# Performance work log

Measured on AMD Instinct MI355X. Metric: run time of the kernel, lower is better.

## Reference

```python
import jax, jax.numpy as jnp
import numpy as np

N = 100000   # nodes
E = 1600000  # edges
EL = 1000000 # label edges
F = 64       # node_features (== LSTM hidden)
S = 64       # second_features
C = 32       # num_classes


def setup_inputs() -> dict:
    key = jax.random.key(0)
    ks = jax.random.split(key, 11)
    sc = 0.05
    return {
        "x": jax.random.normal(ks[0], (N, F), jnp.float32),
        "edge_index": jax.random.randint(ks[1], (2, E), 0, N, jnp.int32),
        "edge_label_index": jax.random.randint(ks[2], (2, EL), 0, N, jnp.int32),
        "W_ih": jax.random.normal(ks[3], (4 * F, F), jnp.float32) * sc,
        "W_hh": jax.random.normal(ks[4], (4 * F, F), jnp.float32) * sc,
        "b_ih": jax.random.normal(ks[5], (4 * F,), jnp.float32) * sc,
        "b_hh": jax.random.normal(ks[6], (4 * F,), jnp.float32) * sc,
        "W1": jax.random.normal(ks[7], (F, S), jnp.float32) * sc,
        "b1": jnp.zeros((S,), jnp.float32),
        "W2": jax.random.normal(ks[8], (S, C), jnp.float32) * sc,
        "b2": jnp.zeros((C,), jnp.float32),
    }


def lstm_step(x, W_ih, W_hh, b_ih, b_hh):
    # seq_len == 1, h0 = c0 = 0, so W_hh contributes nothing but both biases apply.
    gates = x @ W_ih.T + b_ih + b_hh          # [N, 4F], PyTorch gate order i,f,g,o
    i, f, g, o = jnp.split(gates, 4, axis=-1)
    c = jax.nn.sigmoid(i) * jnp.tanh(g)
    return jax.nn.sigmoid(o) * jnp.tanh(c)    # [N, F]


def gcn_conv(h, W, b, row, col, n):
    # PyG GCNConv default: add self-loops, symmetric normalization.
    hw = h @ W                                 # [n, out]
    loop = jnp.arange(n, dtype=row.dtype)
    row_sl = jnp.concatenate([row, loop])
    col_sl = jnp.concatenate([col, loop])
    deg = jax.ops.segment_sum(jnp.ones_like(col_sl, jnp.float32), col_sl, num_segments=n)
    dinv = jnp.where(deg > 0, jax.lax.rsqrt(deg), 0.0)
    norm = dinv[row_sl] * dinv[col_sl]         # [E+n]
    msgs = hw[row_sl] * norm[:, None]          # gather + scale
    out = jax.ops.segment_sum(msgs, col_sl, num_segments=n)  # scatter-add
    return out + b


def reference(x, edge_index, edge_label_index, W_ih, W_hh, b_ih, b_hh, W1, b1, W2, b2):
    n = x.shape[0]
    row, col = edge_index[0], edge_index[1]
    h = lstm_step(x, W_ih, W_hh, b_ih, b_hh)
    h = jax.nn.relu(gcn_conv(h, W1, b1, row, col, n))
    z = gcn_conv(h, W2, b2, row, col, n)       # [n, C]
    src = z[edge_label_index[0]]
    dst = z[edge_label_index[1]]
    return jnp.sum(src * dst, axis=-1)         # [EL]
```

## Files before the change

### kernel.cpp

```cpp
#include <hip/hip_runtime.h>
#include <hip/hip_bf16.h>
#include <hip/hip_fp16.h>
#include <math.h>
#include <stdint.h>

#define NBSH 9
#define CH   4096

typedef _Float16 h2v  __attribute__((ext_vector_type(2)));
typedef _Float16 half8 __attribute__((ext_vector_type(8)));
typedef float    f32x4 __attribute__((ext_vector_type(4)));

__device__ __forceinline__ float fdot2_(unsigned a, unsigned b, float c) {
    return __builtin_amdgcn_fdot2(__builtin_bit_cast(h2v, a),
                                  __builtin_bit_cast(h2v, b), c, false);
}

__device__ __forceinline__ float2 h2f2_(unsigned u) {
    return __half22float2(__builtin_bit_cast(__half2, u));
}

__device__ __forceinline__ float fast_sigmoid(float x) {
    float t = __expf(x);
    return 1.0f - __builtin_amdgcn_rcpf(1.0f + t);
}
__device__ __forceinline__ float fast_tanh(float x) {
    float t = __expf(2.0f * x);
    return 1.0f - 2.0f * __builtin_amdgcn_rcpf(1.0f + t);
}

__global__ __launch_bounds__(256) void k_bhist(const int* __restrict__ col,
        int* __restrict__ bdeg, int E, int nbuck) {
    __shared__ int cnt[256];
    cnt[threadIdx.x] = 0;
    __syncthreads();
    int base = blockIdx.x * CH;
    int end  = base + CH; if (end > E) end = E;
    for (int t = base + (int)threadIdx.x; t < end; t += 256)
        atomicAdd(&cnt[col[t] >> NBSH], 1);
    __syncthreads();
    if ((int)threadIdx.x < nbuck && cnt[threadIdx.x] > 0)
        atomicAdd(&bdeg[threadIdx.x], cnt[threadIdx.x]);
}

__global__ __launch_bounds__(256) void k_bscan(const int* __restrict__ bdeg,
        int* __restrict__ boff, int* __restrict__ gcur, int nbuck, int E) {
    __shared__ int tmp[256];
    int tid = threadIdx.x;
    int v = (tid < nbuck) ? bdeg[tid] : 0;
    tmp[tid] = v;
    __syncthreads();
#pragma unroll
    for (int s = 1; s < 256; s <<= 1) {
        int t = (tid >= s) ? tmp[tid - s] : 0;
        __syncthreads();
        tmp[tid] += t;
        __syncthreads();
    }
    if (tid < nbuck) {
        int o = tmp[tid] - v;
        boff[tid] = o;
        gcur[tid * 16] = o;
    }
    if (tid == 0) boff[nbuck] = E;
}

__global__ __launch_bounds__(256) void k_bin(
    const int* __restrict__ row, const int* __restrict__ col,
    int* __restrict__ gcur, int2* __restrict__ ebuf, int E, int nbuck)
{
    __shared__ int  cnt[256], lofs[256], gbase[256], cur2[256];
    __shared__ int2 stage[CH];
    int tid  = threadIdx.x;
    int base = blockIdx.x * CH;
    int ned  = E - base; if (ned > CH) ned = CH;

    cnt[tid] = 0;
    __syncthreads();

    int r[16], c[16], b[16];
#pragma unroll
    for (int i = 0; i < 16; i++) {
        int idx = i * 256 + tid;
        if (idx < ned) {
            r[i] = row[base + idx];
            c[i] = col[base + idx];
            b[i] = c[i] >> NBSH;
            atomicAdd(&cnt[b[i]], 1);
        } else { r[i] = 0; c[i] = 0; b[i] = -1; }
    }
    __syncthreads();

    int v = cnt[tid];
    lofs[tid] = v;
    __syncthreads();
#pragma unroll
    for (int s = 1; s < 256; s <<= 1) {
        int t = (tid >= s) ? lofs[tid - s] : 0;
        __syncthreads();
        lofs[tid] += t;
        __syncthreads();
    }
    int excl = lofs[tid] - v;
    __syncthreads();
    lofs[tid] = excl;
    cur2[tid] = excl;
    if (tid < nbuck && v > 0)
        gbase[tid] = atomicAdd(&gcur[tid * 16], v);
    __syncthreads();

#pragma unroll
    for (int i = 0; i < 16; i++) {
        if (b[i] >= 0) {
            int p = atomicAdd(&cur2[b[i]], 1);
            stage[p] = make_int2(r[i], c[i]);
        }
    }
    __syncthreads();

    for (int i = tid; i < ned; i += 256) {
        int2 rc = stage[i];
        int bb = rc.y >> NBSH;
        ebuf[gbase[bb] + (i - lofs[bb])] = rc;
    }
}

__global__ __launch_bounds__(512) void k_csr(
    const int2* __restrict__ ebuf, const int* __restrict__ boff,
    int* __restrict__ off, float* __restrict__ dinv,
    int* __restrict__ nbr, int n, int nbuck, int E)
{
    __shared__ int cnt[512], lofs[512];
    int b   = blockIdx.x;
    int tid = threadIdx.x;
    int c0  = b << NBSH;
    int nn  = n - c0; if (nn > 512) nn = 512; if (nn < 0) nn = 0;
    int lo  = boff[b], hi = boff[b + 1];

    cnt[tid] = 0;
    __syncthreads();
    for (int t = lo + tid; t < hi; t += 512)
        atomicAdd(&cnt[ebuf[t].y & 511], 1);
    __syncthreads();

    int v = cnt[tid];
    lofs[tid] = v;
    __syncthreads();
#pragma unroll
    for (int s = 1; s < 512; s <<= 1) {
        int t = (tid >= s) ? lofs[tid - s] : 0;
        __syncthreads();
        lofs[tid] += t;
        __syncthreads();
    }
    int excl = lofs[tid] - v;
    __syncthreads();

    if (tid < nn) {
        off[c0 + tid]  = lo + excl;
        dinv[c0 + tid] = 1.0f / sqrtf((float)(v + 1));
    }
    if (b == nbuck - 1 && tid == 0) off[n] = E;

    cnt[tid] = excl;
    __syncthreads();
    for (int t = lo + tid; t < hi; t += 512) {
        int2 rc = ebuf[t];
        int p = atomicAdd(&cnt[rc.y & 511], 1);
        nbr[lo + p] = rc.x;
    }
}

__global__ void k_tr(const float* __restrict__ Wih, const float* __restrict__ W1,
                     const float* __restrict__ bih, const float* __restrict__ bhh,
                     uint4* __restrict__ B1tab, uint4* __restrict__ B2tab,
                     float* __restrict__ bsum) {
    int t = blockIdx.x * 256 + threadIdx.x;
    if (t < 1536) {
        int e = t >> 6, l = t & 63;
        int tt = e >> 1, kh = e & 1;
        int gate = tt >> 2, tj = tt & 3;
        int j = 16 * tj + (l & 15);
        int rowb = (gate == 0) ? j : (gate == 1) ? (128 + j) : (192 + j);
        int kbase = kh * 32 + 8 * (l >> 4);
        _Float16 v[8];
#pragma unroll
        for (int jj = 0; jj < 8; jj++)
            v[jj] = (_Float16)Wih[rowb * 64 + kbase + jj];
        B1tab[t] = *reinterpret_cast<uint4*>(v);
    } else if (t < 2048) {
        int u = t - 1536;
        int e = u >> 6, l = u & 63;
        int tt = e >> 1, kh = e & 1;
        int s = 16 * tt + (l & 15);
        int kbase = kh * 32 + 8 * (l >> 4);
        _Float16 v[8];
#pragma unroll
        for (int jj = 0; jj < 8; jj++)
            v[jj] = (_Float16)W1[(kbase + jj) * 64 + s];
        B2tab[u] = *reinterpret_cast<uint4*>(v);
    } else if (t < 2240) {
        int c = t - 2048;
        int gate = c >> 6, j = c & 63;
        int rowb = (gate == 0) ? j : (gate == 1) ? (128 + j) : (192 + j);
        bsum[c] = bih[rowb] + bhh[rowb];
    }
}

__global__ __launch_bounds__(256) void k_lstm_mm1(
    const float* __restrict__ x, const uint4* __restrict__ B1tab,
    const uint4* __restrict__ B2tab, const float* __restrict__ bsum,
    __half* __restrict__ hw1, int n)
{
    __shared__ _Float16 hs[4][16 * 72];
    int wv   = threadIdx.x >> 6;
    int lane = threadIdx.x & 63;
    int nbase = (blockIdx.x * 4 + wv) * 16;
    if (nbase >= n) return;
    int m16 = lane & 15, q = lane >> 4;

    int node = nbase + m16; if (node >= n) node = n - 1;
    const float* xr = x + (size_t)node * 64 + 8 * q;
    half8 a0, a1;
#pragma unroll
    for (int jj = 0; jj < 8; jj++) a0[jj] = (_Float16)xr[jj];
#pragma unroll
    for (int jj = 0; jj < 8; jj++) a1[jj] = (_Float16)xr[32 + jj];

    f32x4 c1[12];
#pragma unroll
    for (int t = 0; t < 12; t++) {
        f32x4 acc = {0.f, 0.f, 0.f, 0.f};
        half8 b0 = __builtin_bit_cast(half8, B1tab[(t * 2 + 0) * 64 + lane]);
        half8 b1 = __builtin_bit_cast(half8, B1tab[(t * 2 + 1) * 64 + lane]);
        acc = __builtin_amdgcn_mfma_f32_16x16x32_f16(a0, b0, acc, 0, 0, 0);
        acc = __builtin_amdgcn_mfma_f32_16x16x32_f16(a1, b1, acc, 0, 0, 0);
        c1[t] = acc;
    }

#pragma unroll
    for (int tj = 0; tj < 4; tj++) {
        int j = 16 * tj + m16;
        float bi = bsum[j], bg = bsum[64 + j], bo = bsum[128 + j];
#pragma unroll
        for (int r = 0; r < 4; r++) {
            float gi = c1[tj][r]     + bi;
            float gg = c1[4 + tj][r] + bg;
            float go = c1[8 + tj][r] + bo;
            float cc = fast_sigmoid(gi) * fast_tanh(gg);
            float h  = fast_sigmoid(go) * fast_tanh(cc);
            hs[wv][(q * 4 + r) * 72 + j] = (_Float16)h;
        }
    }

    half8 a20 = __builtin_bit_cast(half8,
        *reinterpret_cast<const uint4*>(&hs[wv][m16 * 72 + 8 * q]));
    half8 a21 = __builtin_bit_cast(half8,
        *reinterpret_cast<const uint4*>(&hs[wv][m16 * 72 + 32 + 8 * q]));

    f32x4 c2[4];
#pragma unroll
    for (int t = 0; t < 4; t++) {
        f32x4 acc = {0.f, 0.f, 0.f, 0.f};
        half8 b0 = __builtin_bit_cast(half8, B2tab[(t * 2 + 0) * 64 + lane]);
        half8 b1 = __builtin_bit_cast(half8, B2tab[(t * 2 + 1) * 64 + lane]);
        acc = __builtin_amdgcn_mfma_f32_16x16x32_f16(a20, b0, acc, 0, 0, 0);
        acc = __builtin_amdgcn_mfma_f32_16x16x32_f16(a21, b1, acc, 0, 0, 0);
        c2[t] = acc;
    }

#pragma unroll
    for (int t = 0; t < 4; t++) {
#pragma unroll
        for (int r = 0; r < 4; r++) {
            int nd = nbase + q * 4 + r;
            if (nd < n)
                hw1[(size_t)nd * 64 + 16 * t + m16] = __float2half(c2[t][r]);
        }
    }
}

__global__ __launch_bounds__(256) void k_pull64(
    const __half* __restrict__ hw, const int* __restrict__ off,
    const int* __restrict__ nbr, const float* __restrict__ dinv,
    const float* __restrict__ b1, float* __restrict__ h1, int n)
{
    int w    = (blockIdx.x * 256 + threadIdx.x) >> 6;
    int lane = threadIdx.x & 63;
    int quad = lane >> 4;
    int fp   = lane & 15;
    if (w * 4 >= n) return;
    int node = w * 4 + quad;
    bool alive = node < n;
    int s = 0, e = 0;
    if (alive) { s = off[node]; e = off[node + 1]; }

    float s0x=0.f,s0y=0.f,s0z=0.f,s0w=0.f;
    float s1x=0.f,s1y=0.f,s1z=0.f,s1w=0.f;
    float s2x=0.f,s2y=0.f,s2z=0.f,s2w=0.f;
    float s3x=0.f,s3y=0.f,s3z=0.f,s3w=0.f;

    for (int base = s; base < e; base += 16) {
        int t = base + fp;
        int idx = 0; float wv = 0.f;
        if (t < e) { idx = nbr[t]; wv = dinv[idx]; }
        int cnt = e - base; if (cnt > 16) cnt = 16;

        int k = 0;
        for (; k + 4 <= cnt; k += 4) {
            int   r0 = __shfl(idx, k + 0, 16); float w0 = __shfl(wv, k + 0, 16);
            int   r1 = __shfl(idx, k + 1, 16); float w1 = __shfl(wv, k + 1, 16);
            int   r2 = __shfl(idx, k + 2, 16); float w2 = __shfl(wv, k + 2, 16);
            int   r3 = __shfl(idx, k + 3, 16); float w3 = __shfl(wv, k + 3, 16);
            uint2 u0 = reinterpret_cast<const uint2*>(hw + (size_t)r0 * 64)[fp];
            uint2 u1 = reinterpret_cast<const uint2*>(hw + (size_t)r1 * 64)[fp];
            uint2 u2 = reinterpret_cast<const uint2*>(hw + (size_t)r2 * 64)[fp];
            uint2 u3 = reinterpret_cast<const uint2*>(hw + (size_t)r3 * 64)[fp];
            float2 l0 = h2f2_(u0.x), h0 = h2f2_(u0.y);
            float2 l1 = h2f2_(u1.x), h1f = h2f2_(u1.y);
            float2 l2 = h2f2_(u2.x), h2 = h2f2_(u2.y);
            float2 l3 = h2f2_(u3.x), h3 = h2f2_(u3.y);
            s0x = fmaf(l0.x, w0, s0x); s0y = fmaf(l0.y, w0, s0y);
            s0z = fmaf(h0.x, w0, s0z); s0w = fmaf(h0.y, w0, s0w);
            s1x = fmaf(l1.x, w1, s1x); s1y = fmaf(l1.y, w1, s1y);
            s1z = fmaf(h1f.x, w1, s1z); s1w = fmaf(h1f.y, w1, s1w);
            s2x = fmaf(l2.x, w2, s2x); s2y = fmaf(l2.y, w2, s2y);
            s2z = fmaf(h2.x, w2, s2z); s2w = fmaf(h2.y, w2, s2w);
            s3x = fmaf(l3.x, w3, s3x); s3y = fmaf(l3.y, w3, s3y);
            s3z = fmaf(h3.x, w3, s3z); s3w = fmaf(h3.y, w3, s3w);
        }
        for (; k < cnt; k++) {
            int   r0 = __shfl(idx, k, 16);
            float w0 = __shfl(wv, k, 16);
            uint2 u0 = reinterpret_cast<const uint2*>(hw + (size_t)r0 * 64)[fp];
            float2 l0 = h2f2_(u0.x), h0 = h2f2_(u0.y);
            s0x = fmaf(l0.x, w0, s0x); s0y = fmaf(l0.y, w0, s0y);
            s0z = fmaf(h0.x, w0, s0z); s0w = fmaf(h0.y, w0, s0w);
        }
    }

    if (alive) {
        float ax = (s0x + s1x) + (s2x + s3x);
        float ay = (s0y + s1y) + (s2y + s3y);
        float az = (s0z + s1z) + (s2z + s3z);
        float aw = (s0w + s1w) + (s2w + s3w);
        float dc = dinv[node];
        uint2 su = reinterpret_cast<const uint2*>(hw + (size_t)node * 64)[fp];
        float2 sl = h2f2_(su.x), sh = h2f2_(su.y);
        float4 bb = reinterpret_cast<const float4*>(b1)[fp];
        float vx = fmaxf(ax * dc + sl.x * dc * dc + bb.x, 0.0f);
        float vy = fmaxf(ay * dc + sl.y * dc * dc + bb.y, 0.0f);
        float vz = fmaxf(az * dc + sh.x * dc * dc + bb.z, 0.0f);
        float vw = fmaxf(aw * dc + sh.y * dc * dc + bb.w, 0.0f);
        reinterpret_cast<float4*>(h1 + (size_t)node * 64)[fp] =
            make_float4(vx, vy, vz, vw);
    }
}

__global__ __launch_bounds__(256) void k_pull32(
    const __half* __restrict__ hw, const int* __restrict__ off,
    const int* __restrict__ nbr, const float* __restrict__ dinv,
    const float* __restrict__ b2, __half* __restrict__ z, int n)
{
    int w    = (blockIdx.x * 256 + threadIdx.x) >> 6;
    int lane = threadIdx.x & 63;
    int quad = lane >> 4;
    int fp   = lane & 15;
    if (w * 4 >= n) return;
    int node = w * 4 + quad;
    bool alive = node < n;
    int s = 0, e = 0;
    if (alive) { s = off[node]; e = off[node + 1]; }

    float ax0 = 0.f, ay0 = 0.f, ax1 = 0.f, ay1 = 0.f;
    float ax2 = 0.f, ay2 = 0.f, ax3 = 0.f, ay3 = 0.f;

    for (int base = s; base < e; base += 16) {
        int t = base + fp;
        int idx = 0; float wv = 0.f;
        if (t < e) { idx = nbr[t]; wv = dinv[idx]; }
        int cnt = e - base; if (cnt > 16) cnt = 16;

        int k = 0;
        for (; k + 4 <= cnt; k += 4) {
            int   r0 = __shfl(idx, k + 0, 16); float w0 = __shfl(wv, k + 0, 16);
            int   r1 = __shfl(idx, k + 1, 16); float w1 = __shfl(wv, k + 1, 16);
            int   r2 = __shfl(idx, k + 2, 16); float w2 = __shfl(wv, k + 2, 16);
            int   r3 = __shfl(idx, k + 3, 16); float w3 = __shfl(wv, k + 3, 16);
            unsigned u0 = reinterpret_cast<const unsigned*>(hw + (size_t)r0 * 32)[fp];
            unsigned u1 = reinterpret_cast<const unsigned*>(hw + (size_t)r1 * 32)[fp];
            unsigned u2 = reinterpret_cast<const unsigned*>(hw + (size_t)r2 * 32)[fp];
            unsigned u3 = reinterpret_cast<const unsigned*>(hw + (size_t)r3 * 32)[fp];
            float2 f0 = h2f2_(u0), f1 = h2f2_(u1), f2 = h2f2_(u2), f3 = h2f2_(u3);
            ax0 = fmaf(f0.x, w0, ax0); ay0 = fmaf(f0.y, w0, ay0);
            ax1 = fmaf(f1.x, w1, ax1); ay1 = fmaf(f1.y, w1, ay1);
            ax2 = fmaf(f2.x, w2, ax2); ay2 = fmaf(f2.y, w2, ay2);
            ax3 = fmaf(f3.x, w3, ax3); ay3 = fmaf(f3.y, w3, ay3);
        }
        for (; k < cnt; k++) {
            int   r0 = __shfl(idx, k, 16);
            float w0 = __shfl(wv, k, 16);
            unsigned u0 = reinterpret_cast<const unsigned*>(hw + (size_t)r0 * 32)[fp];
            float2 f0 = h2f2_(u0);
            ax0 = fmaf(f0.x, w0, ax0); ay0 = fmaf(f0.y, w0, ay0);
        }
    }

    if (alive) {
        float ax = (ax0 + ax1) + (ax2 + ax3);
        float ay = (ay0 + ay1) + (ay2 + ay3);
        float dc = dinv[node];
        unsigned su = reinterpret_cast<const unsigned*>(hw + (size_t)node * 32)[fp];
        float2 sf = h2f2_(su);
        float2 bb = reinterpret_cast<const float2*>(b2)[fp];
        float vx = ax * dc + sf.x * dc * dc + bb.x;
        float vy = ay * dc + sf.y * dc * dc + bb.y;
        __half2 pk(__float2half(vx), __float2half(vy));
        reinterpret_cast<__half2*>(z + (size_t)node * 32)[fp] = pk;
    }
}

__global__ __launch_bounds__(128) void k_mm2(
    const float* __restrict__ h1, const float* __restrict__ W2,
    __half* __restrict__ hw2, int n)
{
    __shared__ float tile[128 * 65];
    int base  = blockIdx.x * 128;
    int nrows = n - base; if (nrows > 128) nrows = 128;

    for (int idx = threadIdx.x; idx < nrows * 64; idx += 128) {
        int r = idx >> 6, c = idx & 63;
        tile[r * 65 + c] = h1[(size_t)base * 64 + idx];
    }
    __syncthreads();

    int node = base + threadIdx.x;
    if (node >= n) return;

    const float* hrow = &tile[threadIdx.x * 65];
    float acc[32];
#pragma unroll
    for (int s = 0; s < 32; s++) acc[s] = 0.0f;

    for (int k = 0; k < 64; k++) {
        float hk = hrow[k];
        const float* w = W2 + (size_t)k * 32;
#pragma unroll
        for (int s = 0; s < 32; s++) acc[s] = fmaf(hk, w[s], acc[s]);
    }

    uint2* op = reinterpret_cast<uint2*>(hw2 + (size_t)node * 32);
#pragma unroll
    for (int q = 0; q < 8; q++) {
        __half2 lo(__float2half(acc[4*q+0]), __float2half(acc[4*q+1]));
        __half2 hi(__float2half(acc[4*q+2]), __float2half(acc[4*q+3]));
        op[q] = make_uint2(__builtin_bit_cast(unsigned, lo),
                           __builtin_bit_cast(unsigned, hi));
    }
}

__global__ void k_dot(const __half* __restrict__ z, const int* __restrict__ src,
                      const int* __restrict__ dst, float* __restrict__ out, int EL)
{
    int e = blockIdx.x * 256 + threadIdx.x;
    if (e >= EL) return;
    const uint4* a = reinterpret_cast<const uint4*>(z + (size_t)src[e] * 32);
    const uint4* b = reinterpret_cast<const uint4*>(z + (size_t)dst[e] * 32);
    float s = 0.0f;
#pragma unroll
    for (int q = 0; q < 4; q++) {
        uint4 av = a[q], bv = b[q];
        s = fdot2_(av.x, bv.x, s);
        s = fdot2_(av.y, bv.y, s);
        s = fdot2_(av.z, bv.z, s);
        s = fdot2_(av.w, bv.w, s);
    }
    out[e] = s;
}

extern "C" void kernel_launch(void* const* d_in, const int* in_sizes, int n_in,
                              void* d_out, int out_size, void* d_ws, size_t ws_size,
                              hipStream_t stream)
{
    const float* x   = (const float*)d_in[0];
    const int*   ei  = (const int*)d_in[1];
    const int*   eli = (const int*)d_in[2];
    const float* Wih = (const float*)d_in[3];
    const float* bih = (const float*)d_in[5];
    const float* bhh = (const float*)d_in[6];
    const float* W1  = (const float*)d_in[7];
    const float* b1  = (const float*)d_in[8];
    const float* W2  = (const float*)d_in[9];
    const float* b2  = (const float*)d_in[10];

    int n  = in_sizes[0] / 64;
    int E  = in_sizes[1] / 2;
    int EL = in_sizes[2] / 2;

    const int* row  = ei;
    const int* col  = ei + E;
    const int* lsrc = eli;
    const int* ldst = eli + EL;
    float* out = (float*)d_out;

    float*    bufA  = (float*)d_ws;
    float*    bufB  = bufA + (size_t)n * 64;
    float*    dinv  = bufB + (size_t)n * 64;
    uintptr_t pal   = ((uintptr_t)(dinv + n) + 15) & ~(uintptr_t)15;
    uint4*    B1tab = (uint4*)pal;
    uint4*    B2tab = B1tab + 1536;
    float*    bsum  = (float*)(B2tab + 512);
    int*      off   = (int*)(bsum + 192);
    int*      nbr   = off + (n + 1);
    int*      bdeg  = nbr + E;
    int*      boff  = bdeg + 256;
    int*      gcur  = boff + 257;
    int2*     ebuf  = (int2*)bufA;
    __half*   hw1h  = (__half*)bufA;
    __half*   hw2h  = (__half*)bufA;
    float*    h1    = bufB;
    __half*   zh    = (__half*)bufB;

    int nbuck   = (n + (1 << NBSH) - 1) >> NBSH;
    int eblocks = (E + CH - 1) / CH;
    dim3 blk(256);

    k_tr<<<dim3(9), blk, 0, stream>>>(Wih, W1, bih, bhh, B1tab, B2tab, bsum);

    hipMemsetAsync(bdeg, 0, 256 * sizeof(int), stream);
    k_bhist<<<dim3(eblocks), blk, 0, stream>>>(col, bdeg, E, nbuck);
    k_bscan<<<dim3(1), blk, 0, stream>>>(bdeg, boff, gcur, nbuck, E);
    k_bin  <<<dim3(eblocks), blk, 0, stream>>>(row, col, gcur, ebuf, E, nbuck);
    k_csr  <<<dim3(nbuck), dim3(512), 0, stream>>>(ebuf, boff, off, dinv, nbr, n, nbuck, E);

    {
        int blocks = (n + 63) / 64;
        k_lstm_mm1<<<dim3(blocks), blk, 0, stream>>>(x, B1tab, B2tab, bsum, hw1h, n);
    }

    {
        int blocks = (n + 15) / 16;
        k_pull64<<<dim3(blocks), blk, 0, stream>>>(hw1h, off, nbr, dinv, b1, h1, n);
    }

    k_mm2<<<dim3((n + 127) / 128), dim3(128), 0, stream>>>(h1, W2, hw2h, n);

    {
        int blocks = (n + 15) / 16;
        k_pull32<<<dim3(blocks), blk, 0, stream>>>(hw2h, off, nbr, dinv, b2, zh, n);
    }

    k_dot<<<dim3((EL + 255) / 256), blk, 0, stream>>>(zh, lsrc, ldst, out, EL);
}
```

Baseline: 198.6 us.

## Merge independent kernels into shared launches and store layer-1 output in fp16

Folds weight-table preparation into the bucket-histogram launch, and runs edge binning and the LSTM+first matmul as two block ranges of a single launch. This cuts launch count and lets independent work overlap on the GPU. The ReLU'd first-layer aggregate is now stored as fp16 instead of fp32, halving its write and its read in the second matmul. The workspace is re-laid out so ebuf no longer aliases the hw1 buffer. The trade-offs are extra precision loss in h1 and a larger shared-memory footprint for the merged binning/LSTM blocks.

```diff
diff --git a/kernel.cpp b/kernel.cpp
--- a/kernel.cpp
+++ b/kernel.cpp
@@ -29,12 +29,50 @@
     return 1.0f - 2.0f * __builtin_amdgcn_rcpf(1.0f + t);
 }
 
-__global__ __launch_bounds__(256) void k_bhist(const int* __restrict__ col,
-        int* __restrict__ bdeg, int E, int nbuck) {
+__global__ __launch_bounds__(256) void k_trh(
+    const float* __restrict__ Wih, const float* __restrict__ W1,
+    const float* __restrict__ bih, const float* __restrict__ bhh,
+    uint4* __restrict__ B1tab, uint4* __restrict__ B2tab,
+    float* __restrict__ bsum,
+    const int* __restrict__ col, int* __restrict__ bdeg, int E, int nbuck)
+{
+    if (blockIdx.x < 9) {
+        int t = blockIdx.x * 256 + threadIdx.x;
+        if (t < 1536) {
+            int e = t >> 6, l = t & 63;
+            int tt = e >> 1, kh = e & 1;
+            int gate = tt >> 2, tj = tt & 3;
+            int j = 16 * tj + (l & 15);
+            int rowb = (gate == 0) ? j : (gate == 1) ? (128 + j) : (192 + j);
+            int kbase = kh * 32 + 8 * (l >> 4);
+            _Float16 v[8];
+#pragma unroll
+            for (int jj = 0; jj < 8; jj++)
+                v[jj] = (_Float16)Wih[rowb * 64 + kbase + jj];
+            B1tab[t] = *reinterpret_cast<uint4*>(v);
+        } else if (t < 2048) {
+            int u = t - 1536;
+            int e = u >> 6, l = u & 63;
+            int tt = e >> 1, kh = e & 1;
+            int s = 16 * tt + (l & 15);
+            int kbase = kh * 32 + 8 * (l >> 4);
+            _Float16 v[8];
+#pragma unroll
+            for (int jj = 0; jj < 8; jj++)
+                v[jj] = (_Float16)W1[(kbase + jj) * 64 + s];
+            B2tab[u] = *reinterpret_cast<uint4*>(v);
+        } else if (t < 2240) {
+            int c = t - 2048;
+            int gate = c >> 6, j = c & 63;
+            int rowb = (gate == 0) ? j : (gate == 1) ? (128 + j) : (192 + j);
+            bsum[c] = bih[rowb] + bhh[rowb];
+        }
+        return;
+    }
     __shared__ int cnt[256];
     cnt[threadIdx.x] = 0;
     __syncthreads();
-    int base = blockIdx.x * CH;
+    int base = (blockIdx.x - 9) * CH;
     int end  = base + CH; if (end > E) end = E;
     for (int t = base + (int)threadIdx.x; t < end; t += 256)
         atomicAdd(&cnt[col[t] >> NBSH], 1);
@@ -65,159 +103,83 @@
     if (tid == 0) boff[nbuck] = E;
 }
 
-__global__ __launch_bounds__(256) void k_bin(
+__global__ __launch_bounds__(256) void k_binl(
     const int* __restrict__ row, const int* __restrict__ col,
-    int* __restrict__ gcur, int2* __restrict__ ebuf, int E, int nbuck)
-{
-    __shared__ int  cnt[256], lofs[256], gbase[256], cur2[256];
-    __shared__ int2 stage[CH];
-    int tid  = threadIdx.x;
-    int base = blockIdx.x * CH;
-    int ned  = E - base; if (ned > CH) ned = CH;
-
-    cnt[tid] = 0;
-    __syncthreads();
-
-    int r[16], c[16], b[16];
-#pragma unroll
-    for (int i = 0; i < 16; i++) {
-        int idx = i * 256 + tid;
-        if (idx < ned) {
-            r[i] = row[base + idx];
-            c[i] = col[base + idx];
-            b[i] = c[i] >> NBSH;
-            atomicAdd(&cnt[b[i]], 1);
-        } else { r[i] = 0; c[i] = 0; b[i] = -1; }
-    }
-    __syncthreads();
-
-    int v = cnt[tid];
-    lofs[tid] = v;
-    __syncthreads();
-#pragma unroll
-    for (int s = 1; s < 256; s <<= 1) {
-        int t = (tid >= s) ? lofs[tid - s] : 0;
-        __syncthreads();
-        lofs[tid] += t;
-        __syncthreads();
-    }
-    int excl = lofs[tid] - v;
-    __syncthreads();
-    lofs[tid] = excl;
-    cur2[tid] = excl;
-    if (tid < nbuck && v > 0)
-        gbase[tid] = atomicAdd(&gcur[tid * 16], v);
-    __syncthreads();
-
-#pragma unroll
-    for (int i = 0; i < 16; i++) {
-        if (b[i] >= 0) {
-            int p = atomicAdd(&cur2[b[i]], 1);
-            stage[p] = make_int2(r[i], c[i]);
-        }
-    }
-    __syncthreads();
-
-    for (int i = tid; i < ned; i += 256) {
-        int2 rc = stage[i];
-        int bb = rc.y >> NBSH;
-        ebuf[gbase[bb] + (i - lofs[bb])] = rc;
-    }
-}
-
-__global__ __launch_bounds__(512) void k_csr(
-    const int2* __restrict__ ebuf, const int* __restrict__ boff,
-    int* __restrict__ off, float* __restrict__ dinv,
-    int* __restrict__ nbr, int n, int nbuck, int E)
-{
-    __shared__ int cnt[512], lofs[512];
-    int b   = blockIdx.x;
-    int tid = threadIdx.x;
-    int c0  = b << NBSH;
-    int nn  = n - c0; if (nn > 512) nn = 512; if (nn < 0) nn = 0;
-    int lo  = boff[b], hi = boff[b + 1];
-
-    cnt[tid] = 0;
-    __syncthreads();
-    for (int t = lo + tid; t < hi; t += 512)
-        atomicAdd(&cnt[ebuf[t].y & 511], 1);
-    __syncthreads();
-
-    int v = cnt[tid];
-    lofs[tid] = v;
-    __syncthreads();
-#pragma unroll
-    for (int s = 1; s < 512; s <<= 1) {
-        int t = (tid >= s) ? lofs[tid - s] : 0;
-        __syncthreads();
-        lofs[tid] += t;
-        __syncthreads();
-    }
-    int excl = lofs[tid] - v;
-    __syncthreads();
-
-    if (tid < nn) {
-        off[c0 + tid]  = lo + excl;
-        dinv[c0 + tid] = 1.0f / sqrtf((float)(v + 1));
-    }
-    if (b == nbuck - 1 && tid == 0) off[n] = E;
-
-    cnt[tid] = excl;
-    __syncthreads();
-    for (int t = lo + tid; t < hi; t += 512) {
-        int2 rc = ebuf[t];
-        int p = atomicAdd(&cnt[rc.y & 511], 1);
-        nbr[lo + p] = rc.x;
-    }
-}
-
-__global__ void k_tr(const float* __restrict__ Wih, const float* __restrict__ W1,
-                     const float* __restrict__ bih, const float* __restrict__ bhh,
-                     uint4* __restrict__ B1tab, uint4* __restrict__ B2tab,
-                     float* __restrict__ bsum) {
-    int t = blockIdx.x * 256 + threadIdx.x;
-    if (t < 1536) {
-        int e = t >> 6, l = t & 63;
-        int tt = e >> 1, kh = e & 1;
-        int gate = tt >> 2, tj = tt & 3;
-        int j = 16 * tj + (l & 15);
-        int rowb = (gate == 0) ? j : (gate == 1) ? (128 + j) : (192 + j);
-        int kbase = kh * 32 + 8 * (l >> 4);
-        _Float16 v[8];
-#pragma unroll
-        for (int jj = 0; jj < 8; jj++)
-            v[jj] = (_Float16)Wih[rowb * 64 + kbase + jj];
-        B1tab[t] = *reinterpret_cast<uint4*>(v);
-    } else if (t < 2048) {
-        int u = t - 1536;
-        int e = u >> 6, l = u & 63;
-        int tt = e >> 1, kh = e & 1;
-        int s = 16 * tt + (l & 15);
-        int kbase = kh * 32 + 8 * (l >> 4);
-        _Float16 v[8];
-#pragma unroll
-        for (int jj = 0; jj < 8; jj++)
-            v[jj] = (_Float16)W1[(kbase + jj) * 64 + s];
-        B2tab[u] = *reinterpret_cast<uint4*>(v);
-    } else if (t < 2240) {
-        int c = t - 2048;
-        int gate = c >> 6, j = c & 63;
-        int rowb = (gate == 0) ? j : (gate == 1) ? (128 + j) : (192 + j);
-        bsum[c] = bih[rowb] + bhh[rowb];
-    }
-}
-
-__global__ __launch_bounds__(256) void k_lstm_mm1(
+    int* __restrict__ gcur, int2* __restrict__ ebuf, int E, int nbuck,
+    int eblocks,
     const float* __restrict__ x, const uint4* __restrict__ B1tab,
     const uint4* __restrict__ B2tab, const float* __restrict__ bsum,
     __half* __restrict__ hw1, int n)
 {
-    __shared__ _Float16 hs[4][16 * 72];
+    __shared__ int pool[9216];
+    if ((int)blockIdx.x < eblocks) {
+        int* cnt  = pool;
+        int* lofs = pool + 256;
+        int* gbase = pool + 512;
+        int* cur2 = pool + 768;
+        int2* stage = (int2*)(pool + 1024);
+        int tid  = threadIdx.x;
+        int base = blockIdx.x * CH;
+        int ned  = E - base; if (ned > CH) ned = CH;
+
+        cnt[tid] = 0;
+        __syncthreads();
+
+        int r[16], c[16], b[16];
+#pragma unroll
+        for (int i = 0; i < 16; i++) {
+            int idx = i * 256 + tid;
+            if (idx < ned) {
+                r[i] = row[base + idx];
+                c[i] = col[base + idx];
+                b[i] = c[i] >> NBSH;
+                atomicAdd(&cnt[b[i]], 1);
+            } else { r[i] = 0; c[i] = 0; b[i] = -1; }
+        }
+        __syncthreads();
+
+        int v = cnt[tid];
+        lofs[tid] = v;
+        __syncthreads();
+#pragma unroll
+        for (int s = 1; s < 256; s <<= 1) {
+            int t = (tid >= s) ? lofs[tid - s] : 0;
+            __syncthreads();
+            lofs[tid] += t;
+            __syncthreads();
+        }
+        int excl = lofs[tid] - v;
+        __syncthreads();
+        lofs[tid] = excl;
+        cur2[tid] = excl;
+        if (tid < nbuck && v > 0)
+            gbase[tid] = atomicAdd(&gcur[tid * 16], v);
+        __syncthreads();
+
+#pragma unroll
+        for (int i = 0; i < 16; i++) {
+            if (b[i] >= 0) {
+                int p = atomicAdd(&cur2[b[i]], 1);
+                stage[p] = make_int2(r[i], c[i]);
+            }
+        }
+        __syncthreads();
+
+        for (int i = tid; i < ned; i += 256) {
+            int2 rc = stage[i];
+            int bb = rc.y >> NBSH;
+            ebuf[gbase[bb] + (i - lofs[bb])] = rc;
+        }
+        return;
+    }
+
+    _Float16* hsp = (_Float16*)pool;
     int wv   = threadIdx.x >> 6;
     int lane = threadIdx.x & 63;
-    int nbase = (blockIdx.x * 4 + wv) * 16;
+    int nbase = (((int)blockIdx.x - eblocks) * 4 + wv) * 16;
     if (nbase >= n) return;
     int m16 = lane & 15, q = lane >> 4;
+    _Float16* hs = hsp + wv * 1152;
 
     int node = nbase + m16; if (node >= n) node = n - 1;
     const float* xr = x + (size_t)node * 64 + 8 * q;
@@ -249,14 +211,14 @@
             float go = c1[8 + tj][r] + bo;
             float cc = fast_sigmoid(gi) * fast_tanh(gg);
             float h  = fast_sigmoid(go) * fast_tanh(cc);
-            hs[wv][(q * 4 + r) * 72 + j] = (_Float16)h;
+            hs[(q * 4 + r) * 72 + j] = (_Float16)h;
         }
     }
 
     half8 a20 = __builtin_bit_cast(half8,
-        *reinterpret_cast<const uint4*>(&hs[wv][m16 * 72 + 8 * q]));
+        *reinterpret_cast<const uint4*>(&hs[m16 * 72 + 8 * q]));
     half8 a21 = __builtin_bit_cast(half8,
-        *reinterpret_cast<const uint4*>(&hs[wv][m16 * 72 + 32 + 8 * q]));
+        *reinterpret_cast<const uint4*>(&hs[m16 * 72 + 32 + 8 * q]));
 
     f32x4 c2[4];
 #pragma unroll
@@ -280,10 +242,56 @@
     }
 }
 
+__global__ __launch_bounds__(512) void k_csr(
+    const int2* __restrict__ ebuf, const int* __restrict__ boff,
+    int* __restrict__ off, float* __restrict__ dinv,
+    int* __restrict__ nbr, int n, int nbuck, int E)
+{
+    __shared__ int cnt[512], lofs[512];
+    int b   = blockIdx.x;
+    int tid = threadIdx.x;
+    int c0  = b << NBSH;
+    int nn  = n - c0; if (nn > 512) nn = 512; if (nn < 0) nn = 0;
+    int lo  = boff[b], hi = boff[b + 1];
+
+    cnt[tid] = 0;
+    __syncthreads();
+    for (int t = lo + tid; t < hi; t += 512)
+        atomicAdd(&cnt[ebuf[t].y & 511], 1);
+    __syncthreads();
+
+    int v = cnt[tid];
+    lofs[tid] = v;
+    __syncthreads();
+#pragma unroll
+    for (int s = 1; s < 512; s <<= 1) {
+        int t = (tid >= s) ? lofs[tid - s] : 0;
+        __syncthreads();
+        lofs[tid] += t;
+        __syncthreads();
+    }
+    int excl = lofs[tid] - v;
+    __syncthreads();
+
+    if (tid < nn) {
+        off[c0 + tid]  = lo + excl;
+        dinv[c0 + tid] = 1.0f / sqrtf((float)(v + 1));
+    }
+    if (b == nbuck - 1 && tid == 0) off[n] = E;
+
+    cnt[tid] = excl;
+    __syncthreads();
+    for (int t = lo + tid; t < hi; t += 512) {
+        int2 rc = ebuf[t];
+        int p = atomicAdd(&cnt[rc.y & 511], 1);
+        nbr[lo + p] = rc.x;
+    }
+}
+
 __global__ __launch_bounds__(256) void k_pull64(
     const __half* __restrict__ hw, const int* __restrict__ off,
     const int* __restrict__ nbr, const float* __restrict__ dinv,
-    const float* __restrict__ b1, float* __restrict__ h1, int n)
+    const float* __restrict__ b1, __half* __restrict__ h1, int n)
 {
     int w    = (blockIdx.x * 256 + threadIdx.x) >> 6;
     int lane = threadIdx.x & 63;
@@ -352,8 +360,11 @@
         float vy = fmaxf(ay * dc + sl.y * dc * dc + bb.y, 0.0f);
         float vz = fmaxf(az * dc + sh.x * dc * dc + bb.z, 0.0f);
         float vw = fmaxf(aw * dc + sh.y * dc * dc + bb.w, 0.0f);
-        reinterpret_cast<float4*>(h1 + (size_t)node * 64)[fp] =
-            make_float4(vx, vy, vz, vw);
+        __half2 p0(__float2half(vx), __float2half(vy));
+        __half2 p1(__float2half(vz), __float2half(vw));
+        uint2 pk = make_uint2(__builtin_bit_cast(unsigned, p0),
+                              __builtin_bit_cast(unsigned, p1));
+        reinterpret_cast<uint2*>(h1 + (size_t)node * 64)[fp] = pk;
     }
 }
 
@@ -421,16 +432,19 @@
 }
 
 __global__ __launch_bounds__(128) void k_mm2(
-    const float* __restrict__ h1, const float* __restrict__ W2,
+    const __half* __restrict__ h1, const float* __restrict__ W2,
     __half* __restrict__ hw2, int n)
 {
     __shared__ float tile[128 * 65];
     int base  = blockIdx.x * 128;
     int nrows = n - base; if (nrows > 128) nrows = 128;
 
-    for (int idx = threadIdx.x; idx < nrows * 64; idx += 128) {
-        int r = idx >> 6, c = idx & 63;
-        tile[r * 65 + c] = h1[(size_t)base * 64 + idx];
+    for (int idx = threadIdx.x; idx < nrows * 32; idx += 128) {
+        int r = idx >> 5, c = idx & 31;
+        __half2 hv = reinterpret_cast<const __half2*>(h1 + (size_t)(base + r) * 64)[c];
+        float2 f = __half22float2(hv);
+        tile[r * 65 + 2 * c]     = f.x;
+        tile[r * 65 + 2 * c + 1] = f.y;
     }
     __syncthreads();
 
@@ -503,47 +517,47 @@
     const int* ldst = eli + EL;
     float* out = (float*)d_out;
 
-    float*    bufA  = (float*)d_ws;
-    float*    bufB  = bufA + (size_t)n * 64;
-    float*    dinv  = bufB + (size_t)n * 64;
-    uintptr_t pal   = ((uintptr_t)(dinv + n) + 15) & ~(uintptr_t)15;
+    float*    base  = (float*)d_ws;
+    int2*     ebuf  = (int2*)base;
+    __half*   hw2h  = (__half*)base;
+    float*    p1    = base + (size_t)E * 2;
+    __half*   hw1h  = (__half*)p1;
+    float*    p2    = p1 + (size_t)n * 32;
+    __half*   h1h   = (__half*)p2;
+    __half*   zh    = (__half*)p2;
+    float*    dinv  = p2 + (size_t)n * 32;
+    int*      off   = (int*)(dinv + n);
+    int*      nbr   = off + (n + 1);
+    uintptr_t pal   = ((uintptr_t)(nbr + E) + 15) & ~(uintptr_t)15;
     uint4*    B1tab = (uint4*)pal;
     uint4*    B2tab = B1tab + 1536;
     float*    bsum  = (float*)(B2tab + 512);
-    int*      off   = (int*)(bsum + 192);
-    int*      nbr   = off + (n + 1);
-    int*      bdeg  = nbr + E;
+    int*      bdeg  = (int*)(bsum + 192);
     int*      boff  = bdeg + 256;
     int*      gcur  = boff + 257;
-    int2*     ebuf  = (int2*)bufA;
-    __half*   hw1h  = (__half*)bufA;
-    __half*   hw2h  = (__half*)bufA;
-    float*    h1    = bufB;
-    __half*   zh    = (__half*)bufB;
 
     int nbuck   = (n + (1 << NBSH) - 1) >> NBSH;
     int eblocks = (E + CH - 1) / CH;
+    int lblocks = (n + 63) / 64;
     dim3 blk(256);
 
-    k_tr<<<dim3(9), blk, 0, stream>>>(Wih, W1, bih, bhh, B1tab, B2tab, bsum);
-
     hipMemsetAsync(bdeg, 0, 256 * sizeof(int), stream);
-    k_bhist<<<dim3(eblocks), blk, 0, stream>>>(col, bdeg, E, nbuck);
+    k_trh<<<dim3(9 + eblocks), blk, 0, stream>>>(
+        Wih, W1, bih, bhh, B1tab, B2tab, bsum, col, bdeg, E, nbuck);
     k_bscan<<<dim3(1), blk, 0, stream>>>(bdeg, boff, gcur, nbuck, E);
-    k_bin  <<<dim3(eblocks), blk, 0, stream>>>(row, col, gcur, ebuf, E, nbuck);
-    k_csr  <<<dim3(nbuck), dim3(512), 0, stream>>>(ebuf, boff, off, dinv, nbr, n, nbuck, E);
-
-    {
-        int blocks = (n + 63) / 64;
-        k_lstm_mm1<<<dim3(blocks), blk, 0, stream>>>(x, B1tab, B2tab, bsum, hw1h, n);
-    }
+
+    k_binl<<<dim3(eblocks + lblocks), blk, 0, stream>>>(
+        row, col, gcur, ebuf, E, nbuck, eblocks,
+        x, B1tab, B2tab, bsum, hw1h, n);
+
+    k_csr<<<dim3(nbuck), dim3(512), 0, stream>>>(ebuf, boff, off, dinv, nbr, n, nbuck, E);
 
     {
         int blocks = (n + 15) / 16;
-        k_pull64<<<dim3(blocks), blk, 0, stream>>>(hw1h, off, nbr, dinv, b1, h1, n);
-    }
-
-    k_mm2<<<dim3((n + 127) / 128), dim3(128), 0, stream>>>(h1, W2, hw2h, n);
+        k_pull64<<<dim3(blocks), blk, 0, stream>>>(hw1h, off, nbr, dinv, b1, h1h, n);
+    }
+
+    k_mm2<<<dim3((n + 127) / 128), dim3(128), 0, stream>>>(h1h, W2, hw2h, n);
 
     {
         int blocks = (n + 15) / 16;
```

Measured after the change: 180.0 us. 1.1x faster.
